# Performance work log

Measured on AMD Instinct MI355X. Metric: run time of the kernel, lower is better.

The kernel has to match this reference:

```python
import jax, jax.numpy as jnp
import numpy as np

EPS = 0.1
MAX_ITER = 100
THRESH = 0.1  # torch code breaks when mean-over-batch L1 change of u < 0.1


def setup_inputs() -> dict:
    key = jax.random.key(0)
    kx, ky = jax.random.split(key)
    x = jax.random.normal(kx, (8, 2048, 64), dtype=jnp.float32)
    y = jax.random.normal(ky, (8, 2048, 64), dtype=jnp.float32)
    return {"x": x, "y": y}


def _sinkhorn(x, y):
    # Squared-L2 cost matrix: C[b,i,j] = sum_d |x[b,i,d] - y[b,j,d]|^2
    C = jnp.sum(jnp.abs(x[:, :, None, :] - y[:, None, :, :]) ** 2, axis=-1)  # [B,P1,P2]
    B, P1 = x.shape[0], x.shape[1]
    P2 = y.shape[1]
    log_mu = jnp.log(jnp.full((B, P1), 1.0 / P1, dtype=C.dtype) + 1e-8)
    log_nu = jnp.log(jnp.full((B, P2), 1.0 / P2, dtype=C.dtype) + 1e-8)

    def M(u, v):
        # (-C + u_i + v_j) / eps
        return (-C + u[:, :, None] + v[:, None, :]) / EPS

    def body(carry, _):
        u, v, done = carry
        u_new = EPS * (log_mu - jax.scipy.special.logsumexp(M(u, v), axis=-1)) + u
        v_new = EPS * (log_nu - jax.scipy.special.logsumexp(M(u_new, v), axis=-2)) + v
        err = jnp.mean(jnp.sum(jnp.abs(u_new - u), axis=-1))
        # Once converged (torch `break`), freeze u, v.
        u_out = jnp.where(done, u, u_new)
        v_out = jnp.where(done, v, v_new)
        done = done | (err < THRESH)
        return (u_out, v_out, done), None

    u0 = jnp.zeros((B, P1), dtype=C.dtype)
    v0 = jnp.zeros((B, P2), dtype=C.dtype)
    (u, v, _), _ = jax.lax.scan(
        jax.checkpoint(body), (u0, v0, jnp.array(False)), None, length=MAX_ITER
    )
    pi = jnp.exp(M(u, v))                 # transport plan [B,P1,P2]
    cost = jnp.sum(pi * C, axis=(-2, -1))  # [B]
    return cost, pi, C


def reference(x, y):
    return _sinkhorn(x, y)
```

## Files before the change

### kernel.cpp

```cpp
#include <hip/hip_runtime.h>
#include <math.h>

#define B 8
#define P 2048
#define D 64
#define EPS 0.1f
#define INVEPS 10.0f
#define MAXIT 100
#define THRESH 0.1f
#define RSLAB 8
#define ROWS_PER_BLK 32
#define NBLK_A (B * P / ROWS_PER_BLK)
#define PLANES (P / ROWS_PER_BLK)

__global__ __launch_bounds__(256) void build_C(const float* __restrict__ x,
                                               const float* __restrict__ y,
                                               float* __restrict__ C) {
    __shared__ float xs[64 * 68];
    __shared__ float ys[64 * 68];
    const int tid = threadIdx.x;
    const int blk = blockIdx.x;
    const int b   = blk >> 10;
    const int rem = blk & 1023;
    const int i0  = (rem >> 5) << 6;
    const int j0  = (rem & 31) << 6;

    const float4* xg = (const float4*)(x + ((size_t)(b * P + i0)) * D);
    const float4* yg = (const float4*)(y + ((size_t)(b * P + j0)) * D);
#pragma unroll
    for (int p = 0; p < 4; ++p) {
        int q = tid + (p << 8);
        int row = q >> 4, c4 = q & 15;
        float4 xv = xg[row * 16 + c4];
        float4 yv = yg[row * 16 + c4];
        float* xd = &xs[row * 68 + (c4 << 2)];
        xd[0] = xv.x; xd[1] = xv.y; xd[2] = xv.z; xd[3] = xv.w;
        float* yd = &ys[row * 68 + (c4 << 2)];
        yd[0] = yv.x; yd[1] = yv.y; yd[2] = yv.z; yd[3] = yv.w;
    }
    __syncthreads();

    const int ti = tid >> 4, tj = tid & 15;
    float acc[4][4] = {};
#pragma unroll 4
    for (int d4 = 0; d4 < 16; ++d4) {
        float4 xa[4], yb[4];
#pragma unroll
        for (int a = 0; a < 4; ++a)
            xa[a] = *(const float4*)&xs[(ti * 4 + a) * 68 + (d4 << 2)];
#pragma unroll
        for (int bb = 0; bb < 4; ++bb)
            yb[bb] = *(const float4*)&ys[(tj * 4 + bb) * 68 + (d4 << 2)];
#pragma unroll
        for (int a = 0; a < 4; ++a)
#pragma unroll
            for (int bb = 0; bb < 4; ++bb) {
                float dx = xa[a].x - yb[bb].x;
                float dy = xa[a].y - yb[bb].y;
                float dz = xa[a].z - yb[bb].z;
                float dw = xa[a].w - yb[bb].w;
                acc[a][bb] += dx * dx + dy * dy + dz * dz + dw * dw;
            }
    }
    size_t base = ((size_t)b * P + (i0 + ti * 4)) * P + (j0 + tj * 4);
#pragma unroll
    for (int a = 0; a < 4; ++a) {
        float4 o = make_float4(acc[a][0], acc[a][1], acc[a][2], acc[a][3]);
        *(float4*)&C[base + (size_t)a * P] = o;
    }
}

__device__ __forceinline__ void lse_push(float z, float& m, float& s) {
    if (z > m) { s = s * __expf(m - z) + 1.0f; m = z; }
    else       { s += __expf(z - m); }
}
__device__ __forceinline__ void lse_merge(float mo, float so, float& m, float& s) {
    float M = fmaxf(m, mo);
    s = s * __expf(m - M) + so * __expf(mo - M);
    m = M;
}

__global__ void init_ws(float* __restrict__ u, float* __restrict__ v,
                        float* __restrict__ errAcc, unsigned* __restrict__ doneArr,
                        float* __restrict__ cost) {
    int idx = blockIdx.x * blockDim.x + threadIdx.x;
    if (idx < B * P) { u[idx] = 0.0f; v[idx] = 0.0f; }
    if (idx < MAXIT) errAcc[idx] = 0.0f;
    if (idx <= MAXIT) doneArr[idx] = 0u;
    if (idx < B) cost[idx] = 0.0f;
}

__global__ __launch_bounds__(512, 4) void iter_rowcol(
        const float* __restrict__ C, const float* __restrict__ vg,
        float* __restrict__ u, float2* __restrict__ part,
        float* __restrict__ errAcc, const unsigned* __restrict__ doneArr, int t) {
    if (doneArr[t]) return;
    __shared__ float sC[RSLAB * P];
    __shared__ float sv[P];
    __shared__ float su[RSLAB];
    __shared__ float serr[8];
    const int tid = threadIdx.x, lane = tid & 63, wid = tid >> 6;
    const int b  = blockIdx.x >> 6;
    const int q  = blockIdx.x & 63;
    const int r0 = q * ROWS_PER_BLK;
    const float* Cb = C + (size_t)b * P * P;
    const float eps_logmu = EPS * logf(1.0f / (float)P + 1e-8f);

    ((float4*)sv)[tid] = ((const float4*)(vg + (size_t)b * P))[tid];

    float4 pf[8];
    {
        const float4* Crow0 = (const float4*)(Cb + (size_t)(r0 + wid) * P);
#pragma unroll
        for (int k = 0; k < 8; ++k) pf[k] = Crow0[lane + (k << 6)];
    }

    float cm[4], cs[4];
#pragma unroll
    for (int k = 0; k < 4; ++k) { cm[k] = -INFINITY; cs[k] = 0.0f; }
    float werr = 0.0f;
    __syncthreads();

#pragma unroll
    for (int sl = 0; sl < 4; ++sl) {
        const int r = r0 + sl * RSLAB + wid;
        float4* lrow = (float4*)&sC[wid * P];
        float rm[4] = {-INFINITY, -INFINITY, -INFINITY, -INFINITY};
        float rs[4] = {0.0f, 0.0f, 0.0f, 0.0f};
#pragma unroll
        for (int k = 0; k < 8; ++k) {
            int it = lane + (k << 6);
            float4 c4 = pf[k];
            lrow[it] = c4;
            float4 v4 = ((const float4*)sv)[it];
            lse_push((v4.x - c4.x) * INVEPS, rm[0], rs[0]);
            lse_push((v4.y - c4.y) * INVEPS, rm[1], rs[1]);
            lse_push((v4.z - c4.z) * INVEPS, rm[2], rs[2]);
            lse_push((v4.w - c4.w) * INVEPS, rm[3], rs[3]);
        }
        lse_merge(rm[1], rs[1], rm[0], rs[0]);
        lse_merge(rm[3], rs[3], rm[2], rs[2]);
        lse_merge(rm[2], rs[2], rm[0], rs[0]);
#pragma unroll
        for (int off = 32; off; off >>= 1) {
            float mo = __shfl_xor(rm[0], off, 64);
            float so = __shfl_xor(rs[0], off, 64);
            lse_merge(mo, so, rm[0], rs[0]);
        }
        float unew = eps_logmu - EPS * (rm[0] + logf(rs[0]));
        if (lane == 0) {
            int gi = b * P + r;
            werr += fabsf(unew - u[gi]);
            u[gi] = unew;
            su[wid] = unew;
        }
        __syncthreads();

        if (sl < 3) {
            const float4* Crown = (const float4*)(Cb + (size_t)(r + RSLAB) * P);
#pragma unroll
            for (int k = 0; k < 8; ++k) pf[k] = Crown[lane + (k << 6)];
        }

#pragma unroll
        for (int rr = 0; rr < RSLAB; ++rr) {
            float ur = su[rr];
            float4 c4 = *(const float4*)&sC[rr * P + (tid << 2)];
            lse_push((ur - c4.x) * INVEPS, cm[0], cs[0]);
            lse_push((ur - c4.y) * INVEPS, cm[1], cs[1]);
            lse_push((ur - c4.z) * INVEPS, cm[2], cs[2]);
            lse_push((ur - c4.w) * INVEPS, cm[3], cs[3]);
        }
        __syncthreads();
    }

    if (lane == 0) serr[wid] = werr;
    __syncthreads();
    if (tid == 0)
        atomicAdd(&errAcc[t], serr[0] + serr[1] + serr[2] + serr[3] +
                              serr[4] + serr[5] + serr[6] + serr[7]);

    float2* pbase = part + ((size_t)q * B + b) * P;
    *(float4*)&pbase[(tid << 2)]     = make_float4(cm[0], cs[0], cm[1], cs[1]);
    *(float4*)&pbase[(tid << 2) + 2] = make_float4(cm[2], cs[2], cm[3], cs[3]);
}

__global__ __launch_bounds__(256) void iter_merge(
        const float2* __restrict__ part, float* __restrict__ vg,
        const float* __restrict__ errAcc, unsigned* __restrict__ doneArr, int t) {
    __shared__ float2 sred[3][64];
    const int tid = threadIdx.x;
    if (blockIdx.x == 0 && tid == 0) {
        doneArr[t + 1] = doneArr[t] | (errAcc[t] < THRESH * (float)B ? 1u : 0u);
    }
    if (doneArr[t]) return;
    const int cl = tid & 63;
    const int g  = tid >> 6;
    const size_t idx = (size_t)blockIdx.x * 64 + cl;
    float m[2] = {-INFINITY, -INFINITY}, s[2] = {0.0f, 0.0f};
#pragma unroll
    for (int k = 0; k < 8; ++k) {
#pragma unroll
        for (int c = 0; c < 2; ++c) {
            int qq = g * 16 + k * 2 + c;
            float2 pk = part[(size_t)qq * (B * P) + idx];
            lse_merge(pk.x, pk.y, m[c], s[c]);
        }
    }
    lse_merge(m[1], s[1], m[0], s[0]);
    if (g) sred[g - 1][cl] = make_float2(m[0], s[0]);
    __syncthreads();
    if (g == 0) {
#pragma unroll
        for (int gg = 0; gg < 3; ++gg) {
            float2 o = sred[gg][cl];
            lse_merge(o.x, o.y, m[0], s[0]);
        }
        const float eps_logmu = EPS * logf(1.0f / (float)P + 1e-8f);
        vg[idx] = eps_logmu - EPS * (m[0] + logf(s[0]));
    }
}

__global__ __launch_bounds__(256) void final_pi_cost(
        const float* __restrict__ C, const float* __restrict__ u,
        const float* __restrict__ vg, float* __restrict__ pi,
        float* __restrict__ cost) {
    __shared__ float sc[B];
    const int tid = threadIdx.x, lane = tid & 63, wid = tid >> 6;
    if (tid < B) sc[tid] = 0.0f;
    __syncthreads();
    const int gw = blockIdx.x * 4 + wid;
    const int rbase = gw * 4;
    if (rbase >= B * P) return;
    const int b = rbase >> 11;
    const float4* vrow = (const float4*)(vg + b * P);
    float acc = 0.0f;
    for (int k = 0; k < 4; ++k) {
        const int r = rbase + k;
        const float ur = u[r];
        const float4* Crow = (const float4*)(C + (size_t)r * P);
        float4* prow = (float4*)(pi + (size_t)r * P);
        for (int it = lane; it < P / 4; it += 64) {
            float4 c4 = Crow[it];
            float4 v4 = vrow[it];
            float4 p4;
            p4.x = __expf((ur + v4.x - c4.x) * INVEPS);
            p4.y = __expf((ur + v4.y - c4.y) * INVEPS);
            p4.z = __expf((ur + v4.z - c4.z) * INVEPS);
            p4.w = __expf((ur + v4.w - c4.w) * INVEPS);
            prow[it] = p4;
            acc += p4.x * c4.x + p4.y * c4.y + p4.z * c4.z + p4.w * c4.w;
        }
    }
#pragma unroll
    for (int off = 32; off; off >>= 1) acc += __shfl_xor(acc, off, 64);
    if (lane == 0) atomicAdd(&sc[b], acc);
    __syncthreads();
    if (tid < B && sc[tid] != 0.0f) atomicAdd(&cost[tid], sc[tid]);
}

extern "C" void kernel_launch(void* const* d_in, const int* in_sizes, int n_in,
                              void* d_out, int out_size, void* d_ws, size_t ws_size,
                              hipStream_t stream) {
    const float* x = (const float*)d_in[0];
    const float* y = (const float*)d_in[1];
    float* out  = (float*)d_out;
    float* cost = out;
    float* pi   = out + 8;
    float* C    = out + 8 + (size_t)B * P * P;

    float2* part = (float2*)pi;

    float* ws      = (float*)d_ws;
    float* u       = ws;
    float* v       = ws + B * P;
    float* errAcc  = ws + 2 * B * P;
    unsigned* doneArr = (unsigned*)(ws + 2 * B * P + 128);

    hipLaunchKernelGGL(build_C, dim3(8 * 32 * 32), dim3(256), 0, stream, x, y, C);
    hipLaunchKernelGGL(init_ws, dim3(64), dim3(256), 0, stream,
                       u, v, errAcc, doneArr, cost);

    for (int t = 0; t < MAXIT; ++t) {
        hipLaunchKernelGGL(iter_rowcol, dim3(NBLK_A), dim3(512), 0, stream,
                           (const float*)C, (const float*)v, u, part,
                           errAcc, (const unsigned*)doneArr, t);
        hipLaunchKernelGGL(iter_merge, dim3(B * P / 64), dim3(256), 0, stream,
                           (const float2*)part, v, (const float*)errAcc,
                           doneArr, t);
    }

    hipLaunchKernelGGL(final_pi_cost, dim3(1024), dim3(256), 0, stream,
                       (const float*)C, (const float*)u, (const float*)v,
                       pi, cost);
}
```

Baseline: 4.373 ms.

## Restructure Sinkhorn row/col pass: per-wave row ownership, branchless base-2 LSE, LDS tree merge

Each wave now processes four consecutive rows of C held in registers and accumulates column log-sum-exp partials for all 2048 columns in registers. This replaces the shared-memory C slab and its per-slab barriers. The column partials from the eight waves are then combined with an LDS tree reduction before a single write of partials per block. The online LSE update becomes branchless and works in base 2 with pre-scaled v and u, using exp2 and log2 intrinsics. The cost is far more registers per thread (64 extra floats for cm/cs), so launch bounds are lowered to 2 blocks per CU, which may cut occupancy and latency hiding.

```diff
diff --git a/kernel.cpp b/kernel.cpp
--- a/kernel.cpp
+++ b/kernel.cpp
@@ -8,10 +8,24 @@
 #define INVEPS 10.0f
 #define MAXIT 100
 #define THRESH 0.1f
-#define RSLAB 8
 #define ROWS_PER_BLK 32
 #define NBLK_A (B * P / ROWS_PER_BLK)
 #define PLANES (P / ROWS_PER_BLK)
+
+#define S2F   14.4269504089f
+#define NS2F (-14.4269504089f)
+#define EPSLN2 0.069314718056f
+
+#if defined(__AMDGCN__) && __has_builtin(__builtin_amdgcn_exp2f)
+#define EXP2F(x) __builtin_amdgcn_exp2f(x)
+#else
+#define EXP2F(x) exp2f(x)
+#endif
+#if defined(__AMDGCN__) && __has_builtin(__builtin_amdgcn_logf)
+#define LOG2F(x) __builtin_amdgcn_logf(x)
+#else
+#define LOG2F(x) log2f(x)
+#endif
 
 __global__ __launch_bounds__(256) void build_C(const float* __restrict__ x,
                                                const float* __restrict__ y,
@@ -70,13 +84,16 @@
     }
 }
 
-__device__ __forceinline__ void lse_push(float z, float& m, float& s) {
-    if (z > m) { s = s * __expf(m - z) + 1.0f; m = z; }
-    else       { s += __expf(z - m); }
-}
-__device__ __forceinline__ void lse_merge(float mo, float so, float& m, float& s) {
+__device__ __forceinline__ void lse_push2(float z, float& m, float& s) {
+    float d = z - m;
+    float w = EXP2F(-fabsf(d));
+    bool gt = d > 0.0f;
+    m = gt ? z : m;
+    s = fmaf(s, gt ? w : 1.0f, gt ? 1.0f : w);
+}
+__device__ __forceinline__ void lse_merge2(float mo, float so, float& m, float& s) {
     float M = fmaxf(m, mo);
-    s = s * __expf(m - M) + so * __expf(mo - M);
+    s = s * EXP2F(m - M) + so * EXP2F(mo - M);
     m = M;
 }
 
@@ -90,14 +107,58 @@
     if (idx < B) cost[idx] = 0.0f;
 }
 
-__global__ __launch_bounds__(512, 4) void iter_rowcol(
+template <bool MORE>
+__device__ __forceinline__ void row_body(
+        const float* __restrict__ Cb, const float* __restrict__ sv,
+        float* __restrict__ u, int b, int r, int lane,
+        float4 (&pf)[8], float (&cm)[8][4], float (&cs)[8][4],
+        float& werr, float eps_logmu) {
+    float rm[4] = {-INFINITY, -INFINITY, -INFINITY, -INFINITY};
+    float rs[4] = {0.0f, 0.0f, 0.0f, 0.0f};
+#pragma unroll
+    for (int k = 0; k < 8; ++k) {
+        float4 c4 = pf[k];
+        float4 v4 = ((const float4*)sv)[lane + (k << 6)];
+        lse_push2(fmaf(c4.x, NS2F, v4.x), rm[0], rs[0]);
+        lse_push2(fmaf(c4.y, NS2F, v4.y), rm[1], rs[1]);
+        lse_push2(fmaf(c4.z, NS2F, v4.z), rm[2], rs[2]);
+        lse_push2(fmaf(c4.w, NS2F, v4.w), rm[3], rs[3]);
+    }
+    lse_merge2(rm[1], rs[1], rm[0], rs[0]);
+    lse_merge2(rm[3], rs[3], rm[2], rs[2]);
+    lse_merge2(rm[2], rs[2], rm[0], rs[0]);
+#pragma unroll
+    for (int off = 32; off; off >>= 1) {
+        float mo = __shfl_xor(rm[0], off, 64);
+        float so = __shfl_xor(rs[0], off, 64);
+        lse_merge2(mo, so, rm[0], rs[0]);
+    }
+    float unew = eps_logmu - EPSLN2 * (rm[0] + LOG2F(rs[0]));
+    if (lane == 0) {
+        int gi = b * P + r;
+        werr += fabsf(unew - u[gi]);
+        u[gi] = unew;
+    }
+    float u2 = unew * S2F;
+    const float4* CrowN = (const float4*)(Cb + (size_t)(r + 1) * P);
+#pragma unroll
+    for (int k = 0; k < 8; ++k) {
+        float4 c4 = pf[k];
+        if (MORE) pf[k] = CrowN[lane + (k << 6)];
+        lse_push2(fmaf(c4.x, NS2F, u2), cm[k][0], cs[k][0]);
+        lse_push2(fmaf(c4.y, NS2F, u2), cm[k][1], cs[k][1]);
+        lse_push2(fmaf(c4.z, NS2F, u2), cm[k][2], cs[k][2]);
+        lse_push2(fmaf(c4.w, NS2F, u2), cm[k][3], cs[k][3]);
+    }
+}
+
+__global__ __launch_bounds__(512, 2) void iter_rowcol(
         const float* __restrict__ C, const float* __restrict__ vg,
         float* __restrict__ u, float2* __restrict__ part,
         float* __restrict__ errAcc, const unsigned* __restrict__ doneArr, int t) {
     if (doneArr[t]) return;
-    __shared__ float sC[RSLAB * P];
     __shared__ float sv[P];
-    __shared__ float su[RSLAB];
+    __shared__ float2 smrg[4][P];
     __shared__ float serr[8];
     const int tid = threadIdx.x, lane = tid & 63, wid = tid >> 6;
     const int b  = blockIdx.x >> 6;
@@ -106,83 +167,107 @@
     const float* Cb = C + (size_t)b * P * P;
     const float eps_logmu = EPS * logf(1.0f / (float)P + 1e-8f);
 
-    ((float4*)sv)[tid] = ((const float4*)(vg + (size_t)b * P))[tid];
+    {
+        float4 vv = ((const float4*)(vg + (size_t)b * P))[tid];
+        vv.x *= S2F; vv.y *= S2F; vv.z *= S2F; vv.w *= S2F;
+        ((float4*)sv)[tid] = vv;
+    }
+
+    float cm[8][4], cs[8][4];
+#pragma unroll
+    for (int k = 0; k < 8; ++k)
+#pragma unroll
+        for (int c = 0; c < 4; ++c) { cm[k][c] = -INFINITY; cs[k][c] = 0.0f; }
 
     float4 pf[8];
     {
-        const float4* Crow0 = (const float4*)(Cb + (size_t)(r0 + wid) * P);
-#pragma unroll
-        for (int k = 0; k < 8; ++k) pf[k] = Crow0[lane + (k << 6)];
-    }
-
-    float cm[4], cs[4];
-#pragma unroll
-    for (int k = 0; k < 4; ++k) { cm[k] = -INFINITY; cs[k] = 0.0f; }
+        const float4* Crow = (const float4*)(Cb + (size_t)(r0 + (wid << 2)) * P);
+#pragma unroll
+        for (int k = 0; k < 8; ++k) pf[k] = Crow[lane + (k << 6)];
+    }
     float werr = 0.0f;
     __syncthreads();
 
-#pragma unroll
-    for (int sl = 0; sl < 4; ++sl) {
-        const int r = r0 + sl * RSLAB + wid;
-        float4* lrow = (float4*)&sC[wid * P];
-        float rm[4] = {-INFINITY, -INFINITY, -INFINITY, -INFINITY};
-        float rs[4] = {0.0f, 0.0f, 0.0f, 0.0f};
-#pragma unroll
-        for (int k = 0; k < 8; ++k) {
-            int it = lane + (k << 6);
-            float4 c4 = pf[k];
-            lrow[it] = c4;
-            float4 v4 = ((const float4*)sv)[it];
-            lse_push((v4.x - c4.x) * INVEPS, rm[0], rs[0]);
-            lse_push((v4.y - c4.y) * INVEPS, rm[1], rs[1]);
-            lse_push((v4.z - c4.z) * INVEPS, rm[2], rs[2]);
-            lse_push((v4.w - c4.w) * INVEPS, rm[3], rs[3]);
-        }
-        lse_merge(rm[1], rs[1], rm[0], rs[0]);
-        lse_merge(rm[3], rs[3], rm[2], rs[2]);
-        lse_merge(rm[2], rs[2], rm[0], rs[0]);
-#pragma unroll
-        for (int off = 32; off; off >>= 1) {
-            float mo = __shfl_xor(rm[0], off, 64);
-            float so = __shfl_xor(rs[0], off, 64);
-            lse_merge(mo, so, rm[0], rs[0]);
-        }
-        float unew = eps_logmu - EPS * (rm[0] + logf(rs[0]));
-        if (lane == 0) {
-            int gi = b * P + r;
-            werr += fabsf(unew - u[gi]);
-            u[gi] = unew;
-            su[wid] = unew;
-        }
-        __syncthreads();
-
-        if (sl < 3) {
-            const float4* Crown = (const float4*)(Cb + (size_t)(r + RSLAB) * P);
-#pragma unroll
-            for (int k = 0; k < 8; ++k) pf[k] = Crown[lane + (k << 6)];
-        }
-
-#pragma unroll
-        for (int rr = 0; rr < RSLAB; ++rr) {
-            float ur = su[rr];
-            float4 c4 = *(const float4*)&sC[rr * P + (tid << 2)];
-            lse_push((ur - c4.x) * INVEPS, cm[0], cs[0]);
-            lse_push((ur - c4.y) * INVEPS, cm[1], cs[1]);
-            lse_push((ur - c4.z) * INVEPS, cm[2], cs[2]);
-            lse_push((ur - c4.w) * INVEPS, cm[3], cs[3]);
-        }
-        __syncthreads();
-    }
+    const int rb = r0 + (wid << 2);
+    row_body<true >(Cb, sv, u, b, rb + 0, lane, pf, cm, cs, werr, eps_logmu);
+    row_body<true >(Cb, sv, u, b, rb + 1, lane, pf, cm, cs, werr, eps_logmu);
+    row_body<true >(Cb, sv, u, b, rb + 2, lane, pf, cm, cs, werr, eps_logmu);
+    row_body<false>(Cb, sv, u, b, rb + 3, lane, pf, cm, cs, werr, eps_logmu);
 
     if (lane == 0) serr[wid] = werr;
+
+    if (wid >= 4) {
+#pragma unroll
+        for (int k = 0; k < 8; ++k) {
+            float2* dst = &smrg[wid - 4][(lane + (k << 6)) << 2];
+            *(float4*)(dst)     = make_float4(cm[k][0], cs[k][0], cm[k][1], cs[k][1]);
+            *(float4*)(dst + 2) = make_float4(cm[k][2], cs[k][2], cm[k][3], cs[k][3]);
+        }
+    }
     __syncthreads();
     if (tid == 0)
         atomicAdd(&errAcc[t], serr[0] + serr[1] + serr[2] + serr[3] +
                               serr[4] + serr[5] + serr[6] + serr[7]);
-
-    float2* pbase = part + ((size_t)q * B + b) * P;
-    *(float4*)&pbase[(tid << 2)]     = make_float4(cm[0], cs[0], cm[1], cs[1]);
-    *(float4*)&pbase[(tid << 2) + 2] = make_float4(cm[2], cs[2], cm[3], cs[3]);
+    if (wid < 4) {
+#pragma unroll
+        for (int k = 0; k < 8; ++k) {
+            const float2* src = &smrg[wid][(lane + (k << 6)) << 2];
+            float4 a  = *(const float4*)(src);
+            float4 bq = *(const float4*)(src + 2);
+            lse_merge2(a.x,  a.y,  cm[k][0], cs[k][0]);
+            lse_merge2(a.z,  a.w,  cm[k][1], cs[k][1]);
+            lse_merge2(bq.x, bq.y, cm[k][2], cs[k][2]);
+            lse_merge2(bq.z, bq.w, cm[k][3], cs[k][3]);
+        }
+    }
+    __syncthreads();
+    if (wid == 2 || wid == 3) {
+#pragma unroll
+        for (int k = 0; k < 8; ++k) {
+            float2* dst = &smrg[wid - 2][(lane + (k << 6)) << 2];
+            *(float4*)(dst)     = make_float4(cm[k][0], cs[k][0], cm[k][1], cs[k][1]);
+            *(float4*)(dst + 2) = make_float4(cm[k][2], cs[k][2], cm[k][3], cs[k][3]);
+        }
+    }
+    __syncthreads();
+    if (wid < 2) {
+#pragma unroll
+        for (int k = 0; k < 8; ++k) {
+            const float2* src = &smrg[wid][(lane + (k << 6)) << 2];
+            float4 a  = *(const float4*)(src);
+            float4 bq = *(const float4*)(src + 2);
+            lse_merge2(a.x,  a.y,  cm[k][0], cs[k][0]);
+            lse_merge2(a.z,  a.w,  cm[k][1], cs[k][1]);
+            lse_merge2(bq.x, bq.y, cm[k][2], cs[k][2]);
+            lse_merge2(bq.z, bq.w, cm[k][3], cs[k][3]);
+        }
+    }
+    __syncthreads();
+    if (wid == 1) {
+#pragma unroll
+        for (int k = 0; k < 8; ++k) {
+            float2* dst = &smrg[0][(lane + (k << 6)) << 2];
+            *(float4*)(dst)     = make_float4(cm[k][0], cs[k][0], cm[k][1], cs[k][1]);
+            *(float4*)(dst + 2) = make_float4(cm[k][2], cs[k][2], cm[k][3], cs[k][3]);
+        }
+    }
+    __syncthreads();
+    if (wid == 0) {
+        float2* pbase = part + ((size_t)q * B + b) * P;
+#pragma unroll
+        for (int k = 0; k < 8; ++k) {
+            const float2* src = &smrg[0][(lane + (k << 6)) << 2];
+            float4 a  = *(const float4*)(src);
+            float4 bq = *(const float4*)(src + 2);
+            lse_merge2(a.x,  a.y,  cm[k][0], cs[k][0]);
+            lse_merge2(a.z,  a.w,  cm[k][1], cs[k][1]);
+            lse_merge2(bq.x, bq.y, cm[k][2], cs[k][2]);
+            lse_merge2(bq.z, bq.w, cm[k][3], cs[k][3]);
+            float2* dst = &pbase[(lane + (k << 6)) << 2];
+            *(float4*)(dst)     = make_float4(cm[k][0], cs[k][0], cm[k][1], cs[k][1]);
+            *(float4*)(dst + 2) = make_float4(cm[k][2], cs[k][2], cm[k][3], cs[k][3]);
+        }
+    }
 }
 
 __global__ __launch_bounds__(256) void iter_merge(
@@ -204,20 +289,20 @@
         for (int c = 0; c < 2; ++c) {
             int qq = g * 16 + k * 2 + c;
             float2 pk = part[(size_t)qq * (B * P) + idx];
-            lse_merge(pk.x, pk.y, m[c], s[c]);
-        }
-    }
-    lse_merge(m[1], s[1], m[0], s[0]);
+            lse_merge2(pk.x, pk.y, m[c], s[c]);
+        }
+    }
+    lse_merge2(m[1], s[1], m[0], s[0]);
     if (g) sred[g - 1][cl] = make_float2(m[0], s[0]);
     __syncthreads();
     if (g == 0) {
 #pragma unroll
         for (int gg = 0; gg < 3; ++gg) {
             float2 o = sred[gg][cl];
-            lse_merge(o.x, o.y, m[0], s[0]);
+            lse_merge2(o.x, o.y, m[0], s[0]);
         }
         const float eps_logmu = EPS * logf(1.0f / (float)P + 1e-8f);
-        vg[idx] = eps_logmu - EPS * (m[0] + logf(s[0]));
+        vg[idx] = eps_logmu - EPSLN2 * (m[0] + LOG2F(s[0]));
     }
 }
 
```

After: 4.493 ms. 1.03x slower.

## Use base-2 branchless LSE, double-buffer C row prefetch, lighter barriers

Applied to the files above, without the earlier changes.

Rewrites the online logsumexp in base 2 with a branchless update that uses a single exp2 per element, folding the 1/eps scale into a pre-scaled v and u. The slab loop becomes a templated body with ping-pong register buffers, so the next C rows are issued before the current slab is processed instead of after the first barrier. __syncthreads is replaced by an inline s_waitcnt lgkmcnt(0) + s_barrier. The aim is to cut transcendental/ALU cost and hide global load latency. The cost is extra register pressure from two 8×float4 buffers under launch_bounds(512,4), and the custom barrier depends on correct ordering of LDS and global accesses.

```diff
diff --git a/kernel.cpp b/kernel.cpp
--- a/kernel.cpp
+++ b/kernel.cpp
@@ -13,6 +13,25 @@
 #define NBLK_A (B * P / ROWS_PER_BLK)
 #define PLANES (P / ROWS_PER_BLK)
 
+#define S2F   14.4269504089f
+#define NS2F (-14.4269504089f)
+#define EPSLN2 0.069314718056f
+
+#if defined(__AMDGCN__) && __has_builtin(__builtin_amdgcn_exp2f)
+#define EXP2F(x) __builtin_amdgcn_exp2f(x)
+#else
+#define EXP2F(x) exp2f(x)
+#endif
+#if defined(__AMDGCN__) && __has_builtin(__builtin_amdgcn_logf)
+#define LOG2F(x) __builtin_amdgcn_logf(x)
+#else
+#define LOG2F(x) log2f(x)
+#endif
+
+__device__ __forceinline__ void block_sync_lgkm() {
+    asm volatile("s_waitcnt lgkmcnt(0)\n\ts_barrier" ::: "memory");
+}
+
 __global__ __launch_bounds__(256) void build_C(const float* __restrict__ x,
                                                const float* __restrict__ y,
                                                float* __restrict__ C) {
@@ -70,13 +89,16 @@
     }
 }
 
-__device__ __forceinline__ void lse_push(float z, float& m, float& s) {
-    if (z > m) { s = s * __expf(m - z) + 1.0f; m = z; }
-    else       { s += __expf(z - m); }
-}
-__device__ __forceinline__ void lse_merge(float mo, float so, float& m, float& s) {
+__device__ __forceinline__ void lse_push2(float z, float& m, float& s) {
+    float d = z - m;
+    float w = EXP2F(-fabsf(d));
+    bool gt = d > 0.0f;
+    m = gt ? z : m;
+    s = fmaf(s, gt ? w : 1.0f, gt ? 1.0f : w);
+}
+__device__ __forceinline__ void lse_merge2(float mo, float so, float& m, float& s) {
     float M = fmaxf(m, mo);
-    s = s * __expf(m - M) + so * __expf(mo - M);
+    s = s * EXP2F(m - M) + so * EXP2F(mo - M);
     m = M;
 }
 
@@ -88,6 +110,60 @@
     if (idx < MAXIT) errAcc[idx] = 0.0f;
     if (idx <= MAXIT) doneArr[idx] = 0u;
     if (idx < B) cost[idx] = 0.0f;
+}
+
+template <bool MORE>
+__device__ __forceinline__ void slab_body(
+        const float* __restrict__ Cb, const float* __restrict__ sv,
+        float* __restrict__ sC, float* __restrict__ su,
+        float* __restrict__ u, int b, int r, int lane, int wid, int tid,
+        float4 (&cur)[8], float4 (&nxt)[8],
+        float (&cm)[4], float (&cs)[4], float& werr, float eps_logmu) {
+    if (MORE) {
+        const float4* CrowN = (const float4*)(Cb + (size_t)(r + RSLAB) * P);
+#pragma unroll
+        for (int k = 0; k < 8; ++k) nxt[k] = CrowN[lane + (k << 6)];
+    }
+    float4* lrow = (float4*)&sC[wid * P];
+    float rm[4] = {-INFINITY, -INFINITY, -INFINITY, -INFINITY};
+    float rs[4] = {0.0f, 0.0f, 0.0f, 0.0f};
+#pragma unroll
+    for (int k = 0; k < 8; ++k) {
+        float4 c4 = cur[k];
+        lrow[lane + (k << 6)] = c4;
+        float4 v4 = ((const float4*)sv)[lane + (k << 6)];
+        lse_push2(fmaf(c4.x, NS2F, v4.x), rm[0], rs[0]);
+        lse_push2(fmaf(c4.y, NS2F, v4.y), rm[1], rs[1]);
+        lse_push2(fmaf(c4.z, NS2F, v4.z), rm[2], rs[2]);
+        lse_push2(fmaf(c4.w, NS2F, v4.w), rm[3], rs[3]);
+    }
+    lse_merge2(rm[1], rs[1], rm[0], rs[0]);
+    lse_merge2(rm[3], rs[3], rm[2], rs[2]);
+    lse_merge2(rm[2], rs[2], rm[0], rs[0]);
+#pragma unroll
+    for (int off = 32; off; off >>= 1) {
+        float mo = __shfl_xor(rm[0], off, 64);
+        float so = __shfl_xor(rs[0], off, 64);
+        lse_merge2(mo, so, rm[0], rs[0]);
+    }
+    float unew = eps_logmu - EPSLN2 * (rm[0] + LOG2F(rs[0]));
+    if (lane == 0) {
+        int gi = b * P + r;
+        werr += fabsf(unew - u[gi]);
+        u[gi] = unew;
+        su[wid] = unew;
+    }
+    block_sync_lgkm();
+#pragma unroll
+    for (int rr = 0; rr < RSLAB; ++rr) {
+        float u2 = su[rr] * S2F;
+        float4 c4 = *(const float4*)&sC[rr * P + (tid << 2)];
+        lse_push2(fmaf(c4.x, NS2F, u2), cm[0], cs[0]);
+        lse_push2(fmaf(c4.y, NS2F, u2), cm[1], cs[1]);
+        lse_push2(fmaf(c4.z, NS2F, u2), cm[2], cs[2]);
+        lse_push2(fmaf(c4.w, NS2F, u2), cm[3], cs[3]);
+    }
+    block_sync_lgkm();
 }
 
 __global__ __launch_bounds__(512, 4) void iter_rowcol(
@@ -106,76 +182,33 @@
     const float* Cb = C + (size_t)b * P * P;
     const float eps_logmu = EPS * logf(1.0f / (float)P + 1e-8f);
 
-    ((float4*)sv)[tid] = ((const float4*)(vg + (size_t)b * P))[tid];
-
-    float4 pf[8];
     {
-        const float4* Crow0 = (const float4*)(Cb + (size_t)(r0 + wid) * P);
-#pragma unroll
-        for (int k = 0; k < 8; ++k) pf[k] = Crow0[lane + (k << 6)];
+        float4 vv = ((const float4*)(vg + (size_t)b * P))[tid];
+        vv.x *= S2F; vv.y *= S2F; vv.z *= S2F; vv.w *= S2F;
+        ((float4*)sv)[tid] = vv;
+    }
+
+    float4 pfA[8], pfB[8];
+    {
+        const float4* Crow = (const float4*)(Cb + (size_t)(r0 + wid) * P);
+#pragma unroll
+        for (int k = 0; k < 8; ++k) pfA[k] = Crow[lane + (k << 6)];
     }
 
     float cm[4], cs[4];
 #pragma unroll
-    for (int k = 0; k < 4; ++k) { cm[k] = -INFINITY; cs[k] = 0.0f; }
+    for (int c = 0; c < 4; ++c) { cm[c] = -INFINITY; cs[c] = 0.0f; }
     float werr = 0.0f;
-    __syncthreads();
-
-#pragma unroll
-    for (int sl = 0; sl < 4; ++sl) {
-        const int r = r0 + sl * RSLAB + wid;
-        float4* lrow = (float4*)&sC[wid * P];
-        float rm[4] = {-INFINITY, -INFINITY, -INFINITY, -INFINITY};
-        float rs[4] = {0.0f, 0.0f, 0.0f, 0.0f};
-#pragma unroll
-        for (int k = 0; k < 8; ++k) {
-            int it = lane + (k << 6);
-            float4 c4 = pf[k];
-            lrow[it] = c4;
-            float4 v4 = ((const float4*)sv)[it];
-            lse_push((v4.x - c4.x) * INVEPS, rm[0], rs[0]);
-            lse_push((v4.y - c4.y) * INVEPS, rm[1], rs[1]);
-            lse_push((v4.z - c4.z) * INVEPS, rm[2], rs[2]);
-            lse_push((v4.w - c4.w) * INVEPS, rm[3], rs[3]);
-        }
-        lse_merge(rm[1], rs[1], rm[0], rs[0]);
-        lse_merge(rm[3], rs[3], rm[2], rs[2]);
-        lse_merge(rm[2], rs[2], rm[0], rs[0]);
-#pragma unroll
-        for (int off = 32; off; off >>= 1) {
-            float mo = __shfl_xor(rm[0], off, 64);
-            float so = __shfl_xor(rs[0], off, 64);
-            lse_merge(mo, so, rm[0], rs[0]);
-        }
-        float unew = eps_logmu - EPS * (rm[0] + logf(rs[0]));
-        if (lane == 0) {
-            int gi = b * P + r;
-            werr += fabsf(unew - u[gi]);
-            u[gi] = unew;
-            su[wid] = unew;
-        }
-        __syncthreads();
-
-        if (sl < 3) {
-            const float4* Crown = (const float4*)(Cb + (size_t)(r + RSLAB) * P);
-#pragma unroll
-            for (int k = 0; k < 8; ++k) pf[k] = Crown[lane + (k << 6)];
-        }
-
-#pragma unroll
-        for (int rr = 0; rr < RSLAB; ++rr) {
-            float ur = su[rr];
-            float4 c4 = *(const float4*)&sC[rr * P + (tid << 2)];
-            lse_push((ur - c4.x) * INVEPS, cm[0], cs[0]);
-            lse_push((ur - c4.y) * INVEPS, cm[1], cs[1]);
-            lse_push((ur - c4.z) * INVEPS, cm[2], cs[2]);
-            lse_push((ur - c4.w) * INVEPS, cm[3], cs[3]);
-        }
-        __syncthreads();
-    }
+    block_sync_lgkm();
+
+    const int rb = r0 + wid;
+    slab_body<true >(Cb, sv, sC, su, u, b, rb,      lane, wid, tid, pfA, pfB, cm, cs, werr, eps_logmu);
+    slab_body<true >(Cb, sv, sC, su, u, b, rb + 8,  lane, wid, tid, pfB, pfA, cm, cs, werr, eps_logmu);
+    slab_body<true >(Cb, sv, sC, su, u, b, rb + 16, lane, wid, tid, pfA, pfB, cm, cs, werr, eps_logmu);
+    slab_body<false>(Cb, sv, sC, su, u, b, rb + 24, lane, wid, tid, pfB, pfA, cm, cs, werr, eps_logmu);
 
     if (lane == 0) serr[wid] = werr;
-    __syncthreads();
+    block_sync_lgkm();
     if (tid == 0)
         atomicAdd(&errAcc[t], serr[0] + serr[1] + serr[2] + serr[3] +
                               serr[4] + serr[5] + serr[6] + serr[7]);
@@ -204,20 +237,20 @@
         for (int c = 0; c < 2; ++c) {
             int qq = g * 16 + k * 2 + c;
             float2 pk = part[(size_t)qq * (B * P) + idx];
-            lse_merge(pk.x, pk.y, m[c], s[c]);
+            lse_merge2(pk.x, pk.y, m[c], s[c]);
         }
     }
-    lse_merge(m[1], s[1], m[0], s[0]);
+    lse_merge2(m[1], s[1], m[0], s[0]);
     if (g) sred[g - 1][cl] = make_float2(m[0], s[0]);
     __syncthreads();
     if (g == 0) {
 #pragma unroll
         for (int gg = 0; gg < 3; ++gg) {
             float2 o = sred[gg][cl];
-            lse_merge(o.x, o.y, m[0], s[0]);
+            lse_merge2(o.x, o.y, m[0], s[0]);
         }
         const float eps_logmu = EPS * logf(1.0f / (float)P + 1e-8f);
-        vg[idx] = eps_logmu - EPS * (m[0] + logf(s[0]));
+        vg[idx] = eps_logmu - EPSLN2 * (m[0] + LOG2F(s[0]));
     }
 }
 
```

New measurement: 6.874 ms. 57.2% more time.
